# Kernel optimization log

Measured on AMD Instinct MI355X. Metric: run time of the kernel, lower is better.

Reference implementation:

```python
import jax, jax.numpy as jnp
import numpy as np

B = 64          # number of graphs in the batch
NK = 262144     # total known (branch) nodes
NC = 262144     # total query (trunk) nodes
F = 3           # in_feats (3D coordinates)
H = 256         # hidden_size
O = 3           # out_feats


def _linear_init(key, fan_in, fan_out):
    s = 1.0 / np.sqrt(fan_in)
    kw, kb = jax.random.split(key)
    w = jax.random.uniform(kw, (fan_in, fan_out), minval=-s, maxval=s, dtype=jnp.float32)
    b = jax.random.uniform(kb, (fan_out,), minval=-s, maxval=s, dtype=jnp.float32)
    return w, b


def _mlp3(x, w0, b0, w1, b1, w2, b2):
    h = jax.nn.relu(x @ w0 + b0)
    h = jax.nn.relu(h @ w1 + b1)
    return h @ w2 + b2


def setup_inputs() -> dict:
    key = jax.random.key(0)
    ks = jax.random.split(key, 12)
    known_nodes = jax.random.normal(ks[0], (NK, F), dtype=jnp.float32)
    nodes = jax.random.normal(ks[1], (NC, F), dtype=jnp.float32)
    known_seg = jnp.sort(jax.random.randint(ks[2], (NK,), 0, B)).astype(jnp.int32)
    coord_seg = jnp.sort(jax.random.randint(ks[3], (NC,), 0, B)).astype(jnp.int32)
    # branch (Node_Classification approximated as 3-layer MLP)
    bw0, bb0 = _linear_init(ks[4], F, H)
    bw1, bb1 = _linear_init(ks[5], H, H)
    bw2, bb2 = _linear_init(ks[6], H, H)
    # trunk
    tw0, tb0 = _linear_init(ks[7], F, H)
    tw1, tb1 = _linear_init(ks[8], H, H)
    tw2, tb2 = _linear_init(ks[9], H, H)
    # out head
    ow0, ob0 = _linear_init(ks[10], H, H)
    ow1, ob1 = _linear_init(ks[11], H, O)
    return dict(known_nodes=known_nodes, nodes=nodes, known_seg=known_seg,
                coord_seg=coord_seg,
                bw0=bw0, bb0=bb0, bw1=bw1, bb1=bb1, bw2=bw2, bb2=bb2,
                tw0=tw0, tb0=tb0, tw1=tw1, tb1=tb1, tw2=tw2, tb2=tb2,
                ow0=ow0, ob0=ob0, ow1=ow1, ob1=ob1)


def reference(known_nodes, nodes, known_seg, coord_seg,
              bw0, bb0, bw1, bb1, bw2, bb2,
              tw0, tb0, tw1, tb1, tw2, tb2,
              ow0, ob0, ow1, ob1):
    # branch: per known-node features [NK, H]
    f = _mlp3(known_nodes, bw0, bb0, bw1, bb1, bw2, bb2)
    # trunk: per query-node features [NC, H]
    c = _mlp3(nodes, tw0, tb0, tw1, tb1, tw2, tb2)
    # c[None]*f[:,None] then mean over query axis == f * segment_mean(c)
    seg_sum = jax.ops.segment_sum(c, coord_seg, num_segments=B)        # [B, H]
    cnt = jax.ops.segment_sum(jnp.ones((c.shape[0], 1), c.dtype), coord_seg,
                              num_segments=B)                          # [B, 1]
    seg_mean = seg_sum / jnp.maximum(cnt, 1.0)
    feat = f * seg_mean[known_seg]                                     # [NK, H]
    h = jax.nn.relu(feat @ ow0 + ob0)
    return h @ ow1 + ob1                                               # [NK, O]
```

## Files before the change

### kernel.cpp

```cpp
#include <hip/hip_runtime.h>

#define HH 256
#define NB 64
#define ROWS 64
#define NTOT 262144
#define THREADS 256

typedef _Float16 half8 __attribute__((ext_vector_type(8)));
typedef _Float16 half4 __attribute__((ext_vector_type(4)));
typedef float f32x4 __attribute__((ext_vector_type(4)));

typedef __attribute__((address_space(1))) const void gas_t;
typedef __attribute__((address_space(3))) void las_t;

__device__ __forceinline__ uint32_t swz(uint32_t r, uint32_t k) {
  return (((r << 9) + (k << 1)) ^ ((r & 7) << 4)) ^ ((r & 8) << 3);
}

__device__ __forceinline__ void stage_slab(const char* __restrict__ g, char* l,
                                           int lane)
{
  const char* gp = g + lane * 16;
#pragma unroll
  for (int c = 0; c < 4; ++c)
    __builtin_amdgcn_global_load_lds((gas_t*)(gp + c * 1024), (las_t*)(l + c * 1024),
                                     16, 0, 0);
}

template<int MODE>
__device__ __forceinline__ void heavy_layer(char* act, char* wpan,
                                            const char* __restrict__ wt3,
                                            const float* __restrict__ bias,
                                            const float* __restrict__ seg_mean,
                                            const int* __restrict__ seg_g, int tid)
{
  const int wid  = tid >> 6;
  const int lane = tid & 63;
  const int lr   = lane & 15;
  const int lg   = lane >> 4;
  const int j0   = wid << 6;
  char* slab = wpan + wid * 12288;
  const char* wsrc = wt3 + wid * 4096;

  f32x4 acc[4][4];
#pragma unroll
  for (int jf = 0; jf < 4; ++jf)
#pragma unroll
    for (int rf = 0; rf < 4; ++rf)
      acc[jf][rf] = (f32x4){0.f, 0.f, 0.f, 0.f};

  stage_slab(wsrc + 0 * 16384, slab + 0 * 4096, lane);
  stage_slab(wsrc + 1 * 16384, slab + 1 * 4096, lane);
  stage_slab(wsrc + 2 * 16384, slab + 2 * 4096, lane);

  half8 a[2][4], b[2][4];

  asm volatile("s_waitcnt vmcnt(8)" ::: "memory");
  __builtin_amdgcn_sched_barrier(0);
#pragma unroll
  for (int rf = 0; rf < 4; ++rf)
    b[0][rf] = *(const half8*)(act + swz(rf * 16 + lr, 0 * 32 + lg * 8));
#pragma unroll
  for (int jf = 0; jf < 4; ++jf)
    a[0][jf] = *(const half8*)(slab + 0 * 4096 + jf * 1024 + lane * 16);

#pragma unroll
  for (int ks = 0; ks < 8; ++ks) {
    const int p = ks & 1;
    if (ks < 7) {
      if (ks < 6) asm volatile("s_waitcnt vmcnt(4)" ::: "memory");
      else        asm volatile("s_waitcnt vmcnt(0)" ::: "memory");
      __builtin_amdgcn_sched_barrier(0);
#pragma unroll
      for (int rf = 0; rf < 4; ++rf)
        b[p ^ 1][rf] = *(const half8*)(act + swz(rf * 16 + lr, (ks + 1) * 32 + lg * 8));
#pragma unroll
      for (int jf = 0; jf < 4; ++jf)
        a[p ^ 1][jf] = *(const half8*)(slab + ((ks + 1) % 3) * 4096 + jf * 1024 + lane * 16);
    }
    __builtin_amdgcn_sched_barrier(0);
#pragma unroll
    for (int jf = 0; jf < 4; ++jf)
#pragma unroll
      for (int rf = 0; rf < 4; ++rf)
        acc[jf][rf] = __builtin_amdgcn_mfma_f32_16x16x32_f16(a[p][jf], b[p][rf], acc[jf][rf], 0, 0, 0);
    __builtin_amdgcn_sched_barrier(0);
    if (ks < 5)
      stage_slab(wsrc + (ks + 3) * 16384, slab + (ks % 3) * 4096, lane);
  }

  int sseg[4];
  if (MODE == 2) {
#pragma unroll
    for (int rf = 0; rf < 4; ++rf) sseg[rf] = seg_g[rf * 16 + lr];
  }

  __syncthreads();

#pragma unroll
  for (int jf = 0; jf < 4; ++jf) {
    f32x4 bj = *(const f32x4*)(bias + j0 + jf * 16 + lg * 4);
#pragma unroll
    for (int rf = 0; rf < 4; ++rf) {
      f32x4 v = acc[jf][rf] + bj;
      if (MODE == 2) {
        f32x4 sm = *(const f32x4*)(seg_mean + sseg[rf] * HH + j0 + jf * 16 + lg * 4);
        v *= sm;
      }
      half4 h;
#pragma unroll
      for (int u = 0; u < 4; ++u) {
        float x = v[u];
        if (MODE == 0) x = fmaxf(x, 0.f);
        h[u] = (_Float16)x;
      }
      *(half4*)(act + swz(rf * 16 + lr, j0 + jf * 16 + lg * 4)) = h;
    }
  }
  __syncthreads();
}

__device__ __forceinline__ void layer1_mfma(char* act, const float* __restrict__ x,
                                            int r0g, const float* __restrict__ W0,
                                            const float* __restrict__ b0, int tid)
{
  const int wid  = tid >> 6;
  const int lane = tid & 63;
  const int lr   = lane & 15;
  const int lg   = lane >> 4;
  const int j0   = wid << 6;

  half8 a[4];
#pragma unroll
  for (int jf = 0; jf < 4; ++jf) {
    half8 v = {0, 0, 0, 0, 0, 0, 0, 0};
    if (lg == 0) {
      int j = j0 + jf * 16 + lr;
      v[0] = (_Float16)W0[j];
      v[1] = (_Float16)W0[HH + j];
      v[2] = (_Float16)W0[2 * HH + j];
    }
    a[jf] = v;
  }

  f32x4 acc[4][4];
#pragma unroll
  for (int jf = 0; jf < 4; ++jf)
#pragma unroll
    for (int rf = 0; rf < 4; ++rf)
      acc[jf][rf] = (f32x4){0.f, 0.f, 0.f, 0.f};

#pragma unroll
  for (int rf = 0; rf < 4; ++rf) {
    half8 b = {0, 0, 0, 0, 0, 0, 0, 0};
    if (lg == 0) {
      const float* xp = x + (size_t)(r0g + rf * 16 + lr) * 3;
      b[0] = (_Float16)xp[0];
      b[1] = (_Float16)xp[1];
      b[2] = (_Float16)xp[2];
    }
#pragma unroll
    for (int jf = 0; jf < 4; ++jf)
      acc[jf][rf] = __builtin_amdgcn_mfma_f32_16x16x32_f16(a[jf], b, acc[jf][rf], 0, 0, 0);
  }

#pragma unroll
  for (int jf = 0; jf < 4; ++jf) {
    f32x4 bj = *(const f32x4*)(b0 + j0 + jf * 16 + lg * 4);
#pragma unroll
    for (int rf = 0; rf < 4; ++rf) {
      f32x4 v = acc[jf][rf] + bj;
      half4 h;
#pragma unroll
      for (int u = 0; u < 4; ++u)
        h[u] = (_Float16)fmaxf(v[u], 0.f);
      *(half4*)(act + swz(rf * 16 + lr, j0 + jf * 16 + lg * 4)) = h;
    }
  }
  __syncthreads();
}

__global__ __launch_bounds__(THREADS, 2)
void trunk_kernel(const float* __restrict__ nodes, const int* __restrict__ coord_seg,
                  const float* __restrict__ tw0, const float* __restrict__ tb0,
                  const char* __restrict__ wt3_1, const float* __restrict__ tb1,
                  float* __restrict__ seg_a)
{
  __shared__ __align__(16) char act[ROWS * HH * 2];
  __shared__ __align__(16) char wpan[4 * 12288];
  const int tid = threadIdx.x;
  const int r0g = blockIdx.x * ROWS;

  layer1_mfma(act, nodes, r0g, tw0, tb0, tid);
  heavy_layer<0>(act, wpan, wt3_1, tb1, nullptr, nullptr, tid);

  {
    const int j = tid;
    const int s_lo = coord_seg[r0g];
    const int s_hi = coord_seg[r0g + ROWS - 1];
    if (s_lo == s_hi) {
      float p = 0.f;
#pragma unroll 8
      for (int r = 0; r < ROWS; ++r)
        p += (float)*(const _Float16*)(act + swz(r, j));
      atomicAdd(&seg_a[s_lo * HH + j], p);
    } else {
      for (int s = s_lo; s <= s_hi; ++s) {
        float p = 0.f;
        for (int r = 0; r < ROWS; ++r)
          if (coord_seg[r0g + r] == s)
            p += (float)*(const _Float16*)(act + swz(r, j));
        atomicAdd(&seg_a[s * HH + j], p);
      }
    }
  }
}

__global__ void segmix_kernel(const float* __restrict__ seg_a,
                              const int* __restrict__ coord_seg,
                              const float* __restrict__ tw2,
                              const float* __restrict__ tb2,
                              float* __restrict__ seg_mean)
{
  const int s = blockIdx.x, j = threadIdx.x;
  int lo = 0, n = NTOT;
  while (n > 0) { int h = n >> 1; int mid = lo + h;
    if (coord_seg[mid] < s) { lo = mid + 1; n -= h + 1; } else n = h; }
  int hi = lo; n = NTOT - lo;
  while (n > 0) { int h = n >> 1; int mid = hi + h;
    if (coord_seg[mid] < s + 1) { hi = mid + 1; n -= h + 1; } else n = h; }
  const float cnt = (float)(hi - lo);
  float acc = cnt * tb2[j];
  for (int i = 0; i < HH; ++i)
    acc = fmaf(seg_a[s * HH + i], tw2[i * HH + j], acc);
  seg_mean[s * HH + j] = acc / fmaxf(cnt, 1.0f);
}

__global__ void dbias_kernel(const float* __restrict__ seg_mean,
                             const float* __restrict__ bb2,
                             const float* __restrict__ ow0,
                             const float* __restrict__ ob0,
                             float* __restrict__ d_s)
{
  const int s = blockIdx.x, j = threadIdx.x;
  float acc = ob0[j];
  for (int i = 0; i < HH; ++i)
    acc = fmaf(bb2[i] * seg_mean[s * HH + i], ow0[i * HH + j], acc);
  d_s[s * HH + j] = acc;
}

__global__ __launch_bounds__(THREADS, 2)
void cfuse_kernel(const float* __restrict__ bw2, const float* __restrict__ seg_mean,
                  const char* __restrict__ wt3_ow0, char* __restrict__ Cbuf)
{
  __shared__ __align__(16) char act[ROWS * HH * 2];
  __shared__ __align__(16) char wpan[4 * 12288];
  const int tid = threadIdx.x;
  const int s  = blockIdx.x >> 2;
  const int kc = blockIdx.x & 3;
  const int k0 = kc * 64;

  {
    const int i = tid;
    const float mi = seg_mean[s * HH + i];
    for (int r = 0; r < ROWS; ++r)
      *(_Float16*)(act + swz(r, i)) = (_Float16)(bw2[(size_t)(k0 + r) * HH + i] * mi);
  }
  __syncthreads();

  const int wid  = tid >> 6;
  const int lane = tid & 63;
  const int lr   = lane & 15;
  const int lg   = lane >> 4;
  const int j0   = wid << 6;
  char* slab = wpan + wid * 12288;
  const char* wsrc = wt3_ow0 + wid * 4096;

  f32x4 acc[4][4];
#pragma unroll
  for (int jf = 0; jf < 4; ++jf)
#pragma unroll
    for (int rf = 0; rf < 4; ++rf)
      acc[jf][rf] = (f32x4){0.f, 0.f, 0.f, 0.f};

  stage_slab(wsrc + 0 * 16384, slab + 0 * 4096, lane);
  stage_slab(wsrc + 1 * 16384, slab + 1 * 4096, lane);
  stage_slab(wsrc + 2 * 16384, slab + 2 * 4096, lane);

  half8 a[2][4], b[2][4];
  asm volatile("s_waitcnt vmcnt(8)" ::: "memory");
  __builtin_amdgcn_sched_barrier(0);
#pragma unroll
  for (int rf = 0; rf < 4; ++rf)
    b[0][rf] = *(const half8*)(act + swz(rf * 16 + lr, 0 * 32 + lg * 8));
#pragma unroll
  for (int jf = 0; jf < 4; ++jf)
    a[0][jf] = *(const half8*)(slab + 0 * 4096 + jf * 1024 + lane * 16);

#pragma unroll
  for (int ks = 0; ks < 8; ++ks) {
    const int p = ks & 1;
    if (ks < 7) {
      if (ks < 6) asm volatile("s_waitcnt vmcnt(4)" ::: "memory");
      else        asm volatile("s_waitcnt vmcnt(0)" ::: "memory");
      __builtin_amdgcn_sched_barrier(0);
#pragma unroll
      for (int rf = 0; rf < 4; ++rf)
        b[p ^ 1][rf] = *(const half8*)(act + swz(rf * 16 + lr, (ks + 1) * 32 + lg * 8));
#pragma unroll
      for (int jf = 0; jf < 4; ++jf)
        a[p ^ 1][jf] = *(const half8*)(slab + ((ks + 1) % 3) * 4096 + jf * 1024 + lane * 16);
    }
    __builtin_amdgcn_sched_barrier(0);
#pragma unroll
    for (int jf = 0; jf < 4; ++jf)
#pragma unroll
      for (int rf = 0; rf < 4; ++rf)
        acc[jf][rf] = __builtin_amdgcn_mfma_f32_16x16x32_f16(a[p][jf], b[p][rf], acc[jf][rf], 0, 0, 0);
    __builtin_amdgcn_sched_barrier(0);
    if (ks < 5)
      stage_slab(wsrc + (ks + 3) * 16384, slab + (ks % 3) * 4096, lane);
  }

  char* dbuf = wpan;
#pragma unroll
  for (int jf = 0; jf < 4; ++jf)
#pragma unroll
    for (int rf = 0; rf < 4; ++rf) {
      const int kl = rf * 16 + lr;
#pragma unroll
      for (int u = 0; u < 4; ++u) {
        const int j = j0 + jf * 16 + lg * 4 + u;
        *(_Float16*)(dbuf + j * 128 + ((kl * 2) ^ ((j & 7) << 4))) = (_Float16)acc[jf][rf][u];
      }
    }
  __syncthreads();

  char* Cdst = Cbuf + (size_t)s * 131072 + (size_t)(kc * 2) * 16384;
#pragma unroll
  for (int c = 0; c < 8; ++c) {
    const uint32_t g = c * 4096 + tid * 16;
    const uint32_t sl = g >> 14;
    const uint32_t aa = g & 16383;
    const uint32_t wq = aa >> 12;
    const uint32_t jjf = (aa >> 10) & 3;
    const uint32_t l  = (aa >> 4) & 63;
    const uint32_t j  = wq * 64 + jjf * 16 + (l & 15);
    const uint32_t kl = sl * 32 + ((l >> 4) << 3);
    uint4 v = *(const uint4*)(dbuf + j * 128 + ((kl * 2) ^ ((j & 7) << 4)));
    *(uint4*)(Cdst + sl * 16384 + aa) = v;
  }
}

__global__ __launch_bounds__(THREADS, 2)
void branch_kernel(const float* __restrict__ known_nodes, const int* __restrict__ known_seg,
                   const float* __restrict__ bw0, const float* __restrict__ bb0,
                   const char* __restrict__ wt3_1, const float* __restrict__ bb1,
                   const char* __restrict__ wt3_2, const float* __restrict__ bb2,
                   const float* __restrict__ seg_mean,
                   const char* __restrict__ wt3_o, const float* __restrict__ ob0,
                   const float* __restrict__ ow1, const float* __restrict__ ob1,
                   const char* __restrict__ Cbuf, const float* __restrict__ d_s,
                   int use_fuse, float* __restrict__ out)
{
  __shared__ __align__(16) char act[ROWS * HH * 2];
  __shared__ __align__(16) char wpan[4 * 12288];
  const int tid = threadIdx.x;
  const int bid = ((int)blockIdx.x & 7) * ((int)gridDim.x >> 3) + ((int)blockIdx.x >> 3);
  const int r0g = bid * ROWS;

  layer1_mfma(act, known_nodes, r0g, bw0, bb0, tid);
  heavy_layer<0>(act, wpan, wt3_1, bb1, nullptr, nullptr, tid);

  const int s_lo = known_seg[r0g];
  const int s_hi = known_seg[r0g + ROWS - 1];
  if (use_fuse && s_lo == s_hi) {
    heavy_layer<0>(act, wpan, Cbuf + (size_t)s_lo * 131072, d_s + s_lo * HH,
                   nullptr, nullptr, tid);
  } else {
    heavy_layer<2>(act, wpan, wt3_2, bb2, seg_mean, known_seg + r0g, tid);
    heavy_layer<0>(act, wpan, wt3_o, ob0, nullptr, nullptr, tid);
  }

  float* ps = (float*)wpan;
  {
    const int r = tid & 63;
    const int q = tid >> 6;
    float o0 = 0.f, o1 = 0.f, o2 = 0.f;
    for (int kk = 0; kk < 64; kk += 8) {
      int k0 = q * 64 + kk;
      half8 h = *(const half8*)(act + swz(r, k0));
#pragma unroll
      for (int u = 0; u < 8; ++u) {
        float a = (float)h[u];
        o0 = fmaf(a, ow1[(k0 + u) * 3 + 0], o0);
        o1 = fmaf(a, ow1[(k0 + u) * 3 + 1], o1);
        o2 = fmaf(a, ow1[(k0 + u) * 3 + 2], o2);
      }
    }
    float* p = ps + q * ROWS * 3;
    p[r * 3 + 0] = o0; p[r * 3 + 1] = o1; p[r * 3 + 2] = o2;
  }
  __syncthreads();
  if (tid < ROWS) {
    const int r = tid;
    float* dst = out + (size_t)(r0g + r) * 3;
#pragma unroll
    for (int c = 0; c < 3; ++c) {
      float o = ob1[c];
#pragma unroll
      for (int q = 0; q < 4; ++q) o += ps[q * ROWS * 3 + r * 3 + c];
      dst[c] = o;
    }
  }
}

struct WPtrs { const float* w[4]; char* wt3[4]; };
__global__ void transpose_kernel(WPtrs p)
{
  const int m = blockIdx.x >> 8;
  const int k = blockIdx.x & 255;
  const int j = threadIdx.x;
  size_t off = (size_t)(k >> 5) * 16384 + (size_t)(j >> 6) * 4096
             + (size_t)((j >> 4) & 3) * 1024
             + (size_t)((((k >> 3) & 3) << 4) | (j & 15)) * 16
             + (size_t)(k & 7) * 2;
  *(_Float16*)(p.wt3[m] + off) = (_Float16)p.w[m][k * HH + j];
}

__global__ void zero_kernel(float* __restrict__ p, int n)
{
  int i = blockIdx.x * blockDim.x + threadIdx.x;
  if (i < n) p[i] = 0.f;
}

extern "C" void kernel_launch(void* const* d_in, const int* in_sizes, int n_in,
                              void* d_out, int out_size, void* d_ws, size_t ws_size,
                              hipStream_t stream)
{
  const float* known_nodes = (const float*)d_in[0];
  const float* nodes       = (const float*)d_in[1];
  const int*   known_seg   = (const int*)d_in[2];
  const int*   coord_seg   = (const int*)d_in[3];
  const float* bw0 = (const float*)d_in[4];
  const float* bb0 = (const float*)d_in[5];
  const float* bw1 = (const float*)d_in[6];
  const float* bb1 = (const float*)d_in[7];
  const float* bw2 = (const float*)d_in[8];
  const float* bb2 = (const float*)d_in[9];
  const float* tw0 = (const float*)d_in[10];
  const float* tb0 = (const float*)d_in[11];
  const float* tw1 = (const float*)d_in[12];
  const float* tb1 = (const float*)d_in[13];
  const float* tw2 = (const float*)d_in[14];
  const float* tb2 = (const float*)d_in[15];
  const float* ow0 = (const float*)d_in[16];
  const float* ob0 = (const float*)d_in[17];
  const float* ow1 = (const float*)d_in[18];
  const float* ob1 = (const float*)d_in[19];

  float* out      = (float*)d_out;
  char* p = (char*)d_ws;
  float* seg_a    = (float*)p;            p += (size_t)NB * HH * 4;
  float* seg_mean = (float*)p;            p += (size_t)NB * HH * 4;
  char* wt3_tw1 = p;  p += (size_t)HH * HH * 2;
  char* wt3_bw1 = p;  p += (size_t)HH * HH * 2;
  char* wt3_bw2 = p;  p += (size_t)HH * HH * 2;
  char* wt3_ow0 = p;  p += (size_t)HH * HH * 2;
  float* d_s    = (float*)p;              p += (size_t)NB * HH * 4;
  char* Cbuf    = p;                      p += (size_t)NB * HH * HH * 2;
  const int use_fuse = ((size_t)(p - (char*)d_ws) <= ws_size) ? 1 : 0;

  WPtrs wp;
  wp.w[0] = tw1; wp.wt3[0] = wt3_tw1;
  wp.w[1] = bw1; wp.wt3[1] = wt3_bw1;
  wp.w[2] = bw2; wp.wt3[2] = wt3_bw2;
  wp.w[3] = ow0; wp.wt3[3] = wt3_ow0;

  transpose_kernel<<<4 * 256, 256, 0, stream>>>(wp);
  zero_kernel<<<(NB * HH + 255) / 256, 256, 0, stream>>>(seg_a, NB * HH);
  trunk_kernel<<<NTOT / ROWS, THREADS, 0, stream>>>(nodes, coord_seg,
                                                    tw0, tb0, wt3_tw1, tb1,
                                                    seg_a);
  segmix_kernel<<<NB, 256, 0, stream>>>(seg_a, coord_seg, tw2, tb2, seg_mean);
  if (use_fuse) {
    dbias_kernel<<<NB, 256, 0, stream>>>(seg_mean, bb2, ow0, ob0, d_s);
    cfuse_kernel<<<NB * 4, THREADS, 0, stream>>>(bw2, seg_mean, wt3_ow0, Cbuf);
  }
  branch_kernel<<<NTOT / ROWS, THREADS, 0, stream>>>(known_nodes, known_seg,
                                                     bw0, bb0, wt3_bw1, bb1, wt3_bw2, bb2,
                                                     seg_mean,
                                                     wt3_ow0, ob0, ow1, ob1,
                                                     Cbuf, d_s, use_fuse,
                                                     out);
}
```

Measured before the change: 222.8 us.

## Fuse output head into last MFMA layer and merge small prep kernels

```diff
diff --git a/kernel.cpp b/kernel.cpp
--- a/kernel.cpp
+++ b/kernel.cpp
@@ -26,6 +26,50 @@
     __builtin_amdgcn_global_load_lds((gas_t*)(gp + c * 1024), (las_t*)(l + c * 1024),
                                      16, 0, 0);
 }
+
+#define HEAVY_MFMA_BODY(act, slab, wsrc)                                        \
+  f32x4 acc[4][4];                                                              \
+  _Pragma("unroll")                                                             \
+  for (int jf = 0; jf < 4; ++jf)                                                \
+    _Pragma("unroll")                                                           \
+    for (int rf = 0; rf < 4; ++rf)                                              \
+      acc[jf][rf] = (f32x4){0.f, 0.f, 0.f, 0.f};                                \
+  stage_slab(wsrc + 0 * 16384, slab + 0 * 4096, lane);                          \
+  stage_slab(wsrc + 1 * 16384, slab + 1 * 4096, lane);                          \
+  stage_slab(wsrc + 2 * 16384, slab + 2 * 4096, lane);                          \
+  half8 a[2][4], b[2][4];                                                       \
+  asm volatile("s_waitcnt vmcnt(8)" ::: "memory");                              \
+  __builtin_amdgcn_sched_barrier(0);                                            \
+  _Pragma("unroll")                                                             \
+  for (int rf = 0; rf < 4; ++rf)                                                \
+    b[0][rf] = *(const half8*)(act + swz(rf * 16 + lr, 0 * 32 + lg * 8));       \
+  _Pragma("unroll")                                                             \
+  for (int jf = 0; jf < 4; ++jf)                                                \
+    a[0][jf] = *(const half8*)(slab + 0 * 4096 + jf * 1024 + lane * 16);        \
+  _Pragma("unroll")                                                             \
+  for (int ks = 0; ks < 8; ++ks) {                                              \
+    const int p = ks & 1;                                                       \
+    if (ks < 7) {                                                               \
+      if (ks < 6) asm volatile("s_waitcnt vmcnt(4)" ::: "memory");              \
+      else        asm volatile("s_waitcnt vmcnt(0)" ::: "memory");              \
+      __builtin_amdgcn_sched_barrier(0);                                        \
+      _Pragma("unroll")                                                         \
+      for (int rf = 0; rf < 4; ++rf)                                            \
+        b[p ^ 1][rf] = *(const half8*)(act + swz(rf * 16 + lr, (ks + 1) * 32 + lg * 8)); \
+      _Pragma("unroll")                                                         \
+      for (int jf = 0; jf < 4; ++jf)                                            \
+        a[p ^ 1][jf] = *(const half8*)(slab + ((ks + 1) % 3) * 4096 + jf * 1024 + lane * 16); \
+    }                                                                           \
+    __builtin_amdgcn_sched_barrier(0);                                          \
+    _Pragma("unroll")                                                           \
+    for (int jf = 0; jf < 4; ++jf)                                              \
+      _Pragma("unroll")                                                         \
+      for (int rf = 0; rf < 4; ++rf)                                            \
+        acc[jf][rf] = __builtin_amdgcn_mfma_f32_16x16x32_f16(a[p][jf], b[p][rf], acc[jf][rf], 0, 0, 0); \
+    __builtin_amdgcn_sched_barrier(0);                                          \
+    if (ks < 5)                                                                 \
+      stage_slab(wsrc + (ks + 3) * 16384, slab + (ks % 3) * 4096, lane);        \
+  }
 
 template<int MODE>
 __device__ __forceinline__ void heavy_layer(char* act, char* wpan,
@@ -42,52 +86,7 @@
   char* slab = wpan + wid * 12288;
   const char* wsrc = wt3 + wid * 4096;
 
-  f32x4 acc[4][4];
-#pragma unroll
-  for (int jf = 0; jf < 4; ++jf)
-#pragma unroll
-    for (int rf = 0; rf < 4; ++rf)
-      acc[jf][rf] = (f32x4){0.f, 0.f, 0.f, 0.f};
-
-  stage_slab(wsrc + 0 * 16384, slab + 0 * 4096, lane);
-  stage_slab(wsrc + 1 * 16384, slab + 1 * 4096, lane);
-  stage_slab(wsrc + 2 * 16384, slab + 2 * 4096, lane);
-
-  half8 a[2][4], b[2][4];
-
-  asm volatile("s_waitcnt vmcnt(8)" ::: "memory");
-  __builtin_amdgcn_sched_barrier(0);
-#pragma unroll
-  for (int rf = 0; rf < 4; ++rf)
-    b[0][rf] = *(const half8*)(act + swz(rf * 16 + lr, 0 * 32 + lg * 8));
-#pragma unroll
-  for (int jf = 0; jf < 4; ++jf)
-    a[0][jf] = *(const half8*)(slab + 0 * 4096 + jf * 1024 + lane * 16);
-
-#pragma unroll
-  for (int ks = 0; ks < 8; ++ks) {
-    const int p = ks & 1;
-    if (ks < 7) {
-      if (ks < 6) asm volatile("s_waitcnt vmcnt(4)" ::: "memory");
-      else        asm volatile("s_waitcnt vmcnt(0)" ::: "memory");
-      __builtin_amdgcn_sched_barrier(0);
-#pragma unroll
-      for (int rf = 0; rf < 4; ++rf)
-        b[p ^ 1][rf] = *(const half8*)(act + swz(rf * 16 + lr, (ks + 1) * 32 + lg * 8));
-#pragma unroll
-      for (int jf = 0; jf < 4; ++jf)
-        a[p ^ 1][jf] = *(const half8*)(slab + ((ks + 1) % 3) * 4096 + jf * 1024 + lane * 16);
-    }
-    __builtin_amdgcn_sched_barrier(0);
-#pragma unroll
-    for (int jf = 0; jf < 4; ++jf)
-#pragma unroll
-      for (int rf = 0; rf < 4; ++rf)
-        acc[jf][rf] = __builtin_amdgcn_mfma_f32_16x16x32_f16(a[p][jf], b[p][rf], acc[jf][rf], 0, 0, 0);
-    __builtin_amdgcn_sched_barrier(0);
-    if (ks < 5)
-      stage_slab(wsrc + (ks + 3) * 16384, slab + (ks % 3) * 4096, lane);
-  }
+  HEAVY_MFMA_BODY(act, slab, wsrc)
 
   int sseg[4];
   if (MODE == 2) {
@@ -118,6 +117,79 @@
     }
   }
   __syncthreads();
+}
+
+__device__ __forceinline__ void heavy_layer_out(char* act, char* wpan,
+                                                const char* __restrict__ wt3,
+                                                const float* __restrict__ bias,
+                                                const float* __restrict__ ow1,
+                                                const float* __restrict__ ob1,
+                                                float* __restrict__ out,
+                                                int r0g, int tid)
+{
+  const int wid  = tid >> 6;
+  const int lane = tid & 63;
+  const int lr   = lane & 15;
+  const int lg   = lane >> 4;
+  const int j0   = wid << 6;
+  char* slab = wpan + wid * 12288;
+  const char* wsrc = wt3 + wid * 4096;
+
+  HEAVY_MFMA_BODY(act, slab, wsrc)
+
+  float o[4][3];
+#pragma unroll
+  for (int rf = 0; rf < 4; ++rf)
+#pragma unroll
+    for (int c = 0; c < 3; ++c) o[rf][c] = 0.f;
+
+#pragma unroll
+  for (int jf = 0; jf < 4; ++jf) {
+    f32x4 bj = *(const f32x4*)(bias + j0 + jf * 16 + lg * 4);
+#pragma unroll
+    for (int u = 0; u < 4; ++u) {
+      const int j = j0 + jf * 16 + lg * 4 + u;
+      const float w0 = ow1[j * 3 + 0], w1 = ow1[j * 3 + 1], w2 = ow1[j * 3 + 2];
+#pragma unroll
+      for (int rf = 0; rf < 4; ++rf) {
+        float x = fmaxf(acc[jf][rf][u] + bj[u], 0.f);
+        o[rf][0] = fmaf(x, w0, o[rf][0]);
+        o[rf][1] = fmaf(x, w1, o[rf][1]);
+        o[rf][2] = fmaf(x, w2, o[rf][2]);
+      }
+    }
+  }
+
+#pragma unroll
+  for (int rf = 0; rf < 4; ++rf)
+#pragma unroll
+    for (int c = 0; c < 3; ++c) {
+      o[rf][c] += __shfl_xor(o[rf][c], 16);
+      o[rf][c] += __shfl_xor(o[rf][c], 32);
+    }
+
+  __syncthreads();
+  float* ps = (float*)wpan;
+  if (lg == 0) {
+#pragma unroll
+    for (int rf = 0; rf < 4; ++rf) {
+      const int r = rf * 16 + lr;
+#pragma unroll
+      for (int c = 0; c < 3; ++c) ps[wid * 192 + r * 3 + c] = o[rf][c];
+    }
+  }
+  __syncthreads();
+  if (tid < ROWS) {
+    const int r = tid;
+    float* dst = out + (size_t)(r0g + r) * 3;
+#pragma unroll
+    for (int c = 0; c < 3; ++c) {
+      float v = ob1[c];
+#pragma unroll
+      for (int w = 0; w < 4; ++w) v += ps[w * 192 + r * 3 + c];
+      dst[c] = v;
+    }
+  }
 }
 
 __device__ __forceinline__ void layer1_mfma(char* act, const float* __restrict__ x,
@@ -216,12 +288,17 @@
   }
 }
 
-__global__ void segmix_kernel(const float* __restrict__ seg_a,
-                              const int* __restrict__ coord_seg,
-                              const float* __restrict__ tw2,
-                              const float* __restrict__ tb2,
-                              float* __restrict__ seg_mean)
-{
+__global__ void segprep_kernel(const float* __restrict__ seg_a,
+                               const int* __restrict__ coord_seg,
+                               const float* __restrict__ tw2,
+                               const float* __restrict__ tb2,
+                               const float* __restrict__ bb2,
+                               const float* __restrict__ ow0,
+                               const float* __restrict__ ob0,
+                               float* __restrict__ seg_mean,
+                               float* __restrict__ d_s)
+{
+  __shared__ float sm[HH];
   const int s = blockIdx.x, j = threadIdx.x;
   int lo = 0, n = NTOT;
   while (n > 0) { int h = n >> 1; int mid = lo + h;
@@ -233,20 +310,14 @@
   float acc = cnt * tb2[j];
   for (int i = 0; i < HH; ++i)
     acc = fmaf(seg_a[s * HH + i], tw2[i * HH + j], acc);
-  seg_mean[s * HH + j] = acc / fmaxf(cnt, 1.0f);
-}
-
-__global__ void dbias_kernel(const float* __restrict__ seg_mean,
-                             const float* __restrict__ bb2,
-                             const float* __restrict__ ow0,
-                             const float* __restrict__ ob0,
-                             float* __restrict__ d_s)
-{
-  const int s = blockIdx.x, j = threadIdx.x;
-  float acc = ob0[j];
+  acc /= fmaxf(cnt, 1.0f);
+  seg_mean[s * HH + j] = acc;
+  sm[j] = acc;
+  __syncthreads();
+  float d = ob0[j];
   for (int i = 0; i < HH; ++i)
-    acc = fmaf(bb2[i] * seg_mean[s * HH + i], ow0[i * HH + j], acc);
-  d_s[s * HH + j] = acc;
+    d = fmaf(bb2[i] * sm[i], ow0[i * HH + j], d);
+  d_s[s * HH + j] = d;
 }
 
 __global__ __launch_bounds__(THREADS, 2)
@@ -276,52 +347,9 @@
   char* slab = wpan + wid * 12288;
   const char* wsrc = wt3_ow0 + wid * 4096;
 
-  f32x4 acc[4][4];
-#pragma unroll
-  for (int jf = 0; jf < 4; ++jf)
-#pragma unroll
-    for (int rf = 0; rf < 4; ++rf)
-      acc[jf][rf] = (f32x4){0.f, 0.f, 0.f, 0.f};
-
-  stage_slab(wsrc + 0 * 16384, slab + 0 * 4096, lane);
-  stage_slab(wsrc + 1 * 16384, slab + 1 * 4096, lane);
-  stage_slab(wsrc + 2 * 16384, slab + 2 * 4096, lane);
-
-  half8 a[2][4], b[2][4];
-  asm volatile("s_waitcnt vmcnt(8)" ::: "memory");
-  __builtin_amdgcn_sched_barrier(0);
-#pragma unroll
-  for (int rf = 0; rf < 4; ++rf)
-    b[0][rf] = *(const half8*)(act + swz(rf * 16 + lr, 0 * 32 + lg * 8));
-#pragma unroll
-  for (int jf = 0; jf < 4; ++jf)
-    a[0][jf] = *(const half8*)(slab + 0 * 4096 + jf * 1024 + lane * 16);
-
-#pragma unroll
-  for (int ks = 0; ks < 8; ++ks) {
-    const int p = ks & 1;
-    if (ks < 7) {
-      if (ks < 6) asm volatile("s_waitcnt vmcnt(4)" ::: "memory");
-      else        asm volatile("s_waitcnt vmcnt(0)" ::: "memory");
-      __builtin_amdgcn_sched_barrier(0);
-#pragma unroll
-      for (int rf = 0; rf < 4; ++rf)
-        b[p ^ 1][rf] = *(const half8*)(act + swz(rf * 16 + lr, (ks + 1) * 32 + lg * 8));
-#pragma unroll
-      for (int jf = 0; jf < 4; ++jf)
-        a[p ^ 1][jf] = *(const half8*)(slab + ((ks + 1) % 3) * 4096 + jf * 1024 + lane * 16);
-    }
-    __builtin_amdgcn_sched_barrier(0);
-#pragma unroll
-    for (int jf = 0; jf < 4; ++jf)
-#pragma unroll
-      for (int rf = 0; rf < 4; ++rf)
-        acc[jf][rf] = __builtin_amdgcn_mfma_f32_16x16x32_f16(a[p][jf], b[p][rf], acc[jf][rf], 0, 0, 0);
-    __builtin_amdgcn_sched_barrier(0);
-    if (ks < 5)
-      stage_slab(wsrc + (ks + 3) * 16384, slab + (ks % 3) * 4096, lane);
-  }
-
+  HEAVY_MFMA_BODY(act, slab, wsrc)
+
+  __syncthreads();
   char* dbuf = wpan;
 #pragma unroll
   for (int jf = 0; jf < 4; ++jf)
@@ -375,63 +403,29 @@
   const int s_lo = known_seg[r0g];
   const int s_hi = known_seg[r0g + ROWS - 1];
   if (use_fuse && s_lo == s_hi) {
-    heavy_layer<0>(act, wpan, Cbuf + (size_t)s_lo * 131072, d_s + s_lo * HH,
-                   nullptr, nullptr, tid);
+    heavy_layer_out(act, wpan, Cbuf + (size_t)s_lo * 131072, d_s + s_lo * HH,
+                    ow1, ob1, out, r0g, tid);
   } else {
     heavy_layer<2>(act, wpan, wt3_2, bb2, seg_mean, known_seg + r0g, tid);
-    heavy_layer<0>(act, wpan, wt3_o, ob0, nullptr, nullptr, tid);
-  }
-
-  float* ps = (float*)wpan;
-  {
-    const int r = tid & 63;
-    const int q = tid >> 6;
-    float o0 = 0.f, o1 = 0.f, o2 = 0.f;
-    for (int kk = 0; kk < 64; kk += 8) {
-      int k0 = q * 64 + kk;
-      half8 h = *(const half8*)(act + swz(r, k0));
-#pragma unroll
-      for (int u = 0; u < 8; ++u) {
-        float a = (float)h[u];
-        o0 = fmaf(a, ow1[(k0 + u) * 3 + 0], o0);
-        o1 = fmaf(a, ow1[(k0 + u) * 3 + 1], o1);
-        o2 = fmaf(a, ow1[(k0 + u) * 3 + 2], o2);
-      }
-    }
-    float* p = ps + q * ROWS * 3;
-    p[r * 3 + 0] = o0; p[r * 3 + 1] = o1; p[r * 3 + 2] = o2;
-  }
-  __syncthreads();
-  if (tid < ROWS) {
-    const int r = tid;
-    float* dst = out + (size_t)(r0g + r) * 3;
-#pragma unroll
-    for (int c = 0; c < 3; ++c) {
-      float o = ob1[c];
-#pragma unroll
-      for (int q = 0; q < 4; ++q) o += ps[q * ROWS * 3 + r * 3 + c];
-      dst[c] = o;
-    }
+    heavy_layer_out(act, wpan, wt3_o, ob0, ow1, ob1, out, r0g, tid);
   }
 }
 
 struct WPtrs { const float* w[4]; char* wt3[4]; };
-__global__ void transpose_kernel(WPtrs p)
+__global__ void transpose_kernel(WPtrs p, float* __restrict__ seg_a)
 {
   const int m = blockIdx.x >> 8;
   const int k = blockIdx.x & 255;
   const int j = threadIdx.x;
+  if (blockIdx.x < 16) {
+    float4 z = {0.f, 0.f, 0.f, 0.f};
+    *(float4*)(seg_a + (size_t)blockIdx.x * 1024 + j * 4) = z;
+  }
   size_t off = (size_t)(k >> 5) * 16384 + (size_t)(j >> 6) * 4096
              + (size_t)((j >> 4) & 3) * 1024
              + (size_t)((((k >> 3) & 3) << 4) | (j & 15)) * 16
              + (size_t)(k & 7) * 2;
   *(_Float16*)(p.wt3[m] + off) = (_Float16)p.w[m][k * HH + j];
-}
-
-__global__ void zero_kernel(float* __restrict__ p, int n)
-{
-  int i = blockIdx.x * blockDim.x + threadIdx.x;
-  if (i < n) p[i] = 0.f;
 }
 
 extern "C" void kernel_launch(void* const* d_in, const int* in_sizes, int n_in,
@@ -477,16 +471,14 @@
   wp.w[2] = bw2; wp.wt3[2] = wt3_bw2;
   wp.w[3] = ow0; wp.wt3[3] = wt3_ow0;
 
-  transpose_kernel<<<4 * 256, 256, 0, stream>>>(wp);
-  zero_kernel<<<(NB * HH + 255) / 256, 256, 0, stream>>>(seg_a, NB * HH);
+  transpose_kernel<<<4 * 256, 256, 0, stream>>>(wp, seg_a);
   trunk_kernel<<<NTOT / ROWS, THREADS, 0, stream>>>(nodes, coord_seg,
                                                     tw0, tb0, wt3_tw1, tb1,
                                                     seg_a);
-  segmix_kernel<<<NB, 256, 0, stream>>>(seg_a, coord_seg, tw2, tb2, seg_mean);
-  if (use_fuse) {
-    dbias_kernel<<<NB, 256, 0, stream>>>(seg_mean, bb2, ow0, ob0, d_s);
+  segprep_kernel<<<NB, 256, 0, stream>>>(seg_a, coord_seg, tw2, tb2,
+                                         bb2, ow0, ob0, seg_mean, d_s);
+  if (use_fuse)
     cfuse_kernel<<<NB * 4, THREADS, 0, stream>>>(bw2, seg_mean, wt3_ow0, Cbuf);
-  }
   branch_kernel<<<NTOT / ROWS, THREADS, 0, stream>>>(known_nodes, known_seg,
                                                      bw0, bb0, wt3_bw1, bb1, wt3_bw2, bb2,
                                                      seg_mean,
```

Result: faster. 202.1 us (-9.3%).
